# Optimization experiments

Hardware: AMD Instinct MI355X
Metric: run time of the kernel (lower is better)

Reference implementation:

```python
import jax, jax.numpy as jnp
import numpy as np

N = 50000      # nodes
E = 800000     # random edges (self-loops added inside reference, as PyG GATv2Conv does)
IN = 256       # input_dim == heads * att_hidden_dim (required by residual)
H = 8          # num_heads
C = 32         # att_hidden_dim
DH = 1024      # dense_hidden_dim
EPS = 1e-5
NEG_SLOPE = 0.2


def setup_inputs() -> dict:
    key = jax.random.key(0)
    ks = jax.random.split(key, 8)
    s = 0.05
    return {
        "x": jax.random.normal(ks[0], (N, IN), jnp.float32),
        "edge_index": jax.random.randint(ks[1], (2, E), 0, N, dtype=jnp.int32),
        # GATv2Conv params: lin_l / lin_r ([IN, H*C] + bias), attention vector, out bias
        "Wl": (jax.random.normal(ks[2], (IN, H * C), jnp.float32) * s),
        "bl": jnp.zeros((H * C,), jnp.float32),
        "Wr": (jax.random.normal(ks[3], (IN, H * C), jnp.float32) * s),
        "br": jnp.zeros((H * C,), jnp.float32),
        "att": (jax.random.normal(ks[4], (H, C), jnp.float32) * s),
        "b_gat": jnp.zeros((H * C,), jnp.float32),
        # LayerNorm 1 (PyG graph-mode) affine params
        "g1": jnp.ones((H * C,), jnp.float32),
        "be1": jnp.zeros((H * C,), jnp.float32),
        # MLP: dense_2 (H*C -> DH), dense_3 (DH -> IN)
        "W2": (jax.random.normal(ks[5], (H * C, DH), jnp.float32) * s),
        "b2": jnp.zeros((DH,), jnp.float32),
        "W3": (jax.random.normal(ks[6], (DH, IN), jnp.float32) * s),
        "b3": jnp.zeros((IN,), jnp.float32),
        # LayerNorm 3 affine params
        "g3": jnp.ones((IN,), jnp.float32),
        "be3": jnp.zeros((IN,), jnp.float32),
    }


def graph_layernorm(x, g, b):
    # torch_geometric.nn.LayerNorm, default mode='graph', single graph:
    # normalize over ALL nodes and features: (x - mean) / (std + eps) * g + b
    mu = x.mean()
    xc = x - mu
    std = jnp.sqrt((xc * xc).mean())
    return (xc / (std + EPS)) * g + b


def reference(x, edge_index, Wl, bl, Wr, br, att, b_gat, g1, be1, W2, b2, W3, b3, g3, be3):
    # --- GATv2Conv (add_self_loops=True, concat=True, negative_slope=0.2) ---
    loops = jnp.arange(N, dtype=edge_index.dtype)
    src = jnp.concatenate([edge_index[0], loops])  # message sources j
    dst = jnp.concatenate([edge_index[1], loops])  # message targets i

    xl = (x @ Wl + bl).reshape(N, H, C)  # source-side transform (lin_l)
    xr = (x @ Wr + br).reshape(N, H, C)  # target-side transform (lin_r)

    # per-edge GATv2 attention: leaky_relu(x_l[j] + x_r[i]) . att
    e = jax.nn.leaky_relu(xl[src] + xr[dst], NEG_SLOPE)   # [E+N, H, C]
    logits = jnp.einsum('ehc,hc->eh', e, att)             # [E+N, H]

    # segment softmax over incoming edges of each target node
    m = jax.ops.segment_max(logits, dst, num_segments=N)  # [N, H]
    p = jnp.exp(logits - m[dst])
    denom = jax.ops.segment_sum(p, dst, num_segments=N)   # [N, H]
    alpha = p / denom[dst]                                # [E+N, H]

    # scatter-add weighted source features
    agg = jax.ops.segment_sum(alpha[:, :, None] * xl[src], dst, num_segments=N)
    gat_out = agg.reshape(N, H * C) + b_gat               # concat heads + bias

    # --- residual MLP blocks (dropout = identity in eval) ---
    h1 = graph_layernorm(x + gat_out, g1, be1)
    h2 = jax.nn.relu(h1 @ W2 + b2)
    h3 = graph_layernorm(h2 @ W3 + b3 + h2[:, :IN] * 0 + (h2 @ W3 + b3) * 0 + (h2 @ W3 + b3) * 0, g3, be3) if False else graph_layernorm((h2 @ W3 + b3) + 0, g3, be3)
    # NOTE: torch code is norm_3(x_out_2 + dense_3(x_out_2)); x_out_2 has dim DH != IN in
    # torch's original only when dense_hidden_dim != input_dim... faithful version below:
    h3 = graph_layernorm(h2 @ W3 + b3, g3, be3)
    return h3
```

## Files before the change

kernel.cpp:

```cpp
#include <hip/hip_runtime.h>
#include <hip/hip_bf16.h>

#define HC 256
#define DHID 1024
#define NEG 0.2f
#define LN_EPS 1e-5f
#define NSLOT 1024

typedef unsigned short u16;
typedef unsigned int u32;
typedef __attribute__((ext_vector_type(8))) short bf16x8;
typedef __attribute__((ext_vector_type(4))) float f32x4;

__device__ __forceinline__ float bf2f(u16 u) {
  union { u32 i; float f; } v; v.i = ((u32)u) << 16; return v.f;
}
__device__ __forceinline__ u16 f2bf(float f) {
  union { float f; u32 i; } v; v.f = f;
  u32 r = v.i + 0x7fffu + ((v.i >> 16) & 1u);
  return (u16)(r >> 16);
}

template<bool A_F32, bool RELU, bool OUT_BF16, bool LN>
__global__ __launch_bounds__(256) void gemm_mfma(
    const float* __restrict__ Af, const u16* __restrict__ Ab,
    const u16* __restrict__ BT, const float* __restrict__ bias,
    void* __restrict__ outp, double* __restrict__ sl,
    int M, int K, int NB)
{
  __shared__ __align__(16) u16 As[128][72];
  __shared__ __align__(16) u16 Bs[128][72];
  const int tid = threadIdx.x;
  const int wid = tid >> 6, lane = tid & 63;
  const int rowBase = blockIdx.x * 128;
  const int colBase = blockIdx.y * 128;
  const int wr = (wid >> 1) * 64, wc = (wid & 1) * 64;
  f32x4 acc[4][4] = {};

  for (int k0 = 0; k0 < K; k0 += 64) {
#pragma unroll
    for (int s = 0; s < 4; ++s) {
      const int L = tid + s * 256;
      const int r = L >> 3, cb = (L & 7) << 3;
      const int gr = rowBase + r;
      bf16x8 v = {};
      if (A_F32) {
        if (gr < M) {
          const float* p = &Af[(size_t)gr * K + k0 + cb];
          float4 f0 = *(const float4*)p;
          float4 f1 = *(const float4*)(p + 4);
          v[0] = (short)f2bf(f0.x); v[1] = (short)f2bf(f0.y);
          v[2] = (short)f2bf(f0.z); v[3] = (short)f2bf(f0.w);
          v[4] = (short)f2bf(f1.x); v[5] = (short)f2bf(f1.y);
          v[6] = (short)f2bf(f1.z); v[7] = (short)f2bf(f1.w);
        }
      } else {
        if (gr < M) v = *(const bf16x8*)&Ab[(size_t)gr * K + k0 + cb];
      }
      *(bf16x8*)&As[r][cb] = v;
    }
#pragma unroll
    for (int s = 0; s < 4; ++s) {
      const int L = tid + s * 256;
      const int r = L >> 3, cb = (L & 7) << 3;
      *(bf16x8*)&Bs[r][cb] = *(const bf16x8*)&BT[(size_t)(colBase + r) * K + k0 + cb];
    }
    __syncthreads();
#pragma unroll
    for (int kk = 0; kk < 2; ++kk) {
      bf16x8 af[4], bfr[4];
#pragma unroll
      for (int mr = 0; mr < 4; ++mr)
        af[mr] = *(const bf16x8*)&As[wr + mr * 16 + (lane & 15)][kk * 32 + (lane >> 4) * 8];
#pragma unroll
      for (int nc = 0; nc < 4; ++nc)
        bfr[nc] = *(const bf16x8*)&Bs[wc + nc * 16 + (lane & 15)][kk * 32 + (lane >> 4) * 8];
#pragma unroll
      for (int mr = 0; mr < 4; ++mr)
#pragma unroll
        for (int nc = 0; nc < 4; ++nc)
          acc[mr][nc] = __builtin_amdgcn_mfma_f32_16x16x32_bf16(af[mr], bfr[nc], acc[mr][nc], 0, 0, 0);
    }
    __syncthreads();
  }

  u16* ob = (u16*)outp;
  float* of = (float*)outp;
  const int crow = (lane >> 4) * 4;
  const int ccol = lane & 15;
  float s1 = 0.f, s2 = 0.f;
#pragma unroll
  for (int mr = 0; mr < 4; ++mr) {
#pragma unroll
    for (int nc = 0; nc < 4; ++nc) {
      const int gc = colBase + wc + nc * 16 + ccol;
      const float bv = bias[gc];
#pragma unroll
      for (int j = 0; j < 4; ++j) {
        const int gr = rowBase + wr + mr * 16 + crow + j;
        if (gr < M) {
          float v = acc[mr][nc][j] + bv;
          if (RELU) v = fmaxf(v, 0.f);
          if (OUT_BF16) {
            ob[(size_t)gr * NB + gc] = f2bf(v);
          } else {
            of[(size_t)gr * NB + gc] = v;
            s1 += v; s2 += v * v;
          }
        }
      }
    }
  }
  if (LN) {
#pragma unroll
    for (int d = 1; d < 64; d <<= 1) {
      s1 += __shfl_xor(s1, d);
      s2 += __shfl_xor(s2, d);
    }
    if (lane == 0) {
      int slot = ((blockIdx.x + blockIdx.y * 397) * 4 + wid) & (NSLOT - 1);
      atomicAdd(&sl[slot * 2 + 0], (double)s1);
      atomicAdd(&sl[slot * 2 + 1], (double)s2);
    }
  }
}

__global__ __launch_bounds__(256) void transpose_bf16(
    const float* __restrict__ W, const float* __restrict__ scale,
    u16* __restrict__ WT, int K, int NB)
{
  __shared__ float T[32][33];
  const int k0 = blockIdx.x * 32, n0 = blockIdx.y * 32;
  const int tx = threadIdx.x & 31, ty = threadIdx.x >> 5;
#pragma unroll
  for (int i = 0; i < 32; i += 8) {
    float v = W[(size_t)(k0 + ty + i) * NB + n0 + tx];
    if (scale) v *= scale[k0 + ty + i];
    T[ty + i][tx] = v;
  }
  __syncthreads();
#pragma unroll
  for (int i = 0; i < 32; i += 8)
    WT[(size_t)(n0 + ty + i) * K + k0 + tx] = f2bf(T[tx][ty + i]);
}

__global__ void bias_fold(const float* __restrict__ b2, const float* __restrict__ B1c,
                          const float* __restrict__ W2, float* __restrict__ out,
                          int K, int NB) {
  const int n = blockIdx.x * blockDim.x + threadIdx.x;
  if (n < NB) {
    float s = b2[n];
    for (int k = 0; k < K; ++k) s = fmaf(B1c[k], W2[(size_t)k * NB + n], s);
    out[n] = s;
  }
}

__global__ void deg_count(const int* __restrict__ dst, int* __restrict__ deg, int E) {
  int i = blockIdx.x * blockDim.x + threadIdx.x;
  if (i < E) atomicAdd(&deg[dst[i]], 1);
}

__global__ __launch_bounds__(1024) void scan_k(const int* __restrict__ deg, int* __restrict__ off, int n) {
  __shared__ int wsum[16];
  __shared__ int carrySh;
  const int tid = threadIdx.x, lane = tid & 63, w = tid >> 6;
  if (tid == 0) carrySh = 0;
  __syncthreads();
  for (int base = 0; base < n; base += 1024) {
    int i = base + tid;
    int v = (i < n) ? deg[i] : 0;
    int incl = v;
#pragma unroll
    for (int d = 1; d < 64; d <<= 1) {
      int t = __shfl_up(incl, d);
      if (lane >= d) incl += t;
    }
    if (lane == 63) wsum[w] = incl;
    __syncthreads();
    int waveOff = 0, total = 0;
#pragma unroll
    for (int k = 0; k < 16; ++k) {
      int s = wsum[k];
      if (k < w) waveOff += s;
      total += s;
    }
    int carry = carrySh;
    if (i < n) off[i] = carry + waveOff + incl - v;
    __syncthreads();
    if (tid == 0) carrySh = carry + total;
    __syncthreads();
  }
  if (threadIdx.x == 0) off[n] = carrySh;
}

__global__ void fill_csr(const int* __restrict__ src, const int* __restrict__ dst,
                         const int* __restrict__ off, int* __restrict__ cur,
                         int* __restrict__ csr, int E) {
  int i = blockIdx.x * blockDim.x + threadIdx.x;
  if (i < E) {
    int d = dst[i];
    int pos = off[d] + atomicAdd(&cur[d], 1);
    csr[pos] = src[i];
  }
}

__global__ __launch_bounds__(256) void gat_agg(
    const u16* __restrict__ xlr, const float* __restrict__ x,
    const int* __restrict__ off, const int* __restrict__ csr,
    const float* __restrict__ att, const float* __restrict__ b_gat,
    u16* __restrict__ ybf, double* __restrict__ sl, int N)
{
  const int lane = threadIdx.x & 63;
  const int node = blockIdx.x * 4 + (threadIdx.x >> 6);
  if (node >= N) return;
  const int v0 = lane << 2;
  float attv[4];
  *(float4*)attv = *(const float4*)&att[v0];
  float xrv[4];
  {
    ushort4 u = *(const ushort4*)&xlr[(size_t)node * 512 + 256 + v0];
    xrv[0] = bf2f(u.x); xrv[1] = bf2f(u.y); xrv[2] = bf2f(u.z); xrv[3] = bf2f(u.w);
  }
  float m_run, d_run = 1.f;
  float agg[4];
  {
    ushort4 u = *(const ushort4*)&xlr[(size_t)node * 512 + v0];
    float xlv[4] = {bf2f(u.x), bf2f(u.y), bf2f(u.z), bf2f(u.w)};
    float part = 0.f;
#pragma unroll
    for (int m = 0; m < 4; ++m) {
      float s = xlv[m] + xrv[m];
      s = (s > 0.f) ? s : NEG * s;
      part = fmaf(attv[m], s, part);
    }
    part += __shfl_xor(part, 1);
    part += __shfl_xor(part, 2);
    part += __shfl_xor(part, 4);
    m_run = part;
#pragma unroll
    for (int m = 0; m < 4; ++m) agg[m] = xlv[m];
  }
  const int beg = off[node];
  const int cntE = off[node + 1] - beg;
  for (int e0 = 0; e0 < cntE; e0 += 8) {
    const int nb = cntE - e0;
    int jj[8];
#pragma unroll
    for (int t = 0; t < 8; ++t)
      jj[t] = (t < nb) ? csr[beg + e0 + t] : node;
    ushort4 u[8];
#pragma unroll
    for (int t = 0; t < 8; ++t)
      u[t] = *(const ushort4*)&xlr[(size_t)jj[t] * 512 + v0];
    float lg[8];
#pragma unroll
    for (int t = 0; t < 8; ++t) {
      float part = 0.f;
#pragma unroll
      for (int m = 0; m < 4; ++m) {
        float xv = bf2f(((const u16*)&u[t])[m]);
        float s = xv + xrv[m];
        s = (s > 0.f) ? s : NEG * s;
        part = fmaf(attv[m], s, part);
      }
      part += __shfl_xor(part, 1);
      part += __shfl_xor(part, 2);
      part += __shfl_xor(part, 4);
      lg[t] = (t < nb) ? part : -INFINITY;
    }
    float mb = lg[0];
#pragma unroll
    for (int t = 1; t < 8; ++t) mb = fmaxf(mb, lg[t]);
    const float m_new = fmaxf(m_run, mb);
    const float r = __expf(m_run - m_new);
    d_run *= r;
#pragma unroll
    for (int m = 0; m < 4; ++m) agg[m] *= r;
#pragma unroll
    for (int t = 0; t < 8; ++t) {
      float p = __expf(lg[t] - m_new);
      d_run += p;
#pragma unroll
      for (int m = 0; m < 4; ++m)
        agg[m] = fmaf(p, bf2f(((const u16*)&u[t])[m]), agg[m]);
    }
    m_run = m_new;
  }
  const float inv = 1.f / d_run;
  float xv[4], bg[4];
  *(float4*)xv = *(const float4*)&x[(size_t)node * HC + v0];
  *(float4*)bg = *(const float4*)&b_gat[v0];
  float s1 = 0.f, s2 = 0.f;
  ushort4 ov;
  {
    float v0f = fmaf(agg[0], inv, bg[0]) + xv[0];
    float v1f = fmaf(agg[1], inv, bg[1]) + xv[1];
    float v2f = fmaf(agg[2], inv, bg[2]) + xv[2];
    float v3f = fmaf(agg[3], inv, bg[3]) + xv[3];
    s1 = v0f + v1f + v2f + v3f;
    s2 = v0f * v0f + v1f * v1f + v2f * v2f + v3f * v3f;
    ov.x = f2bf(v0f); ov.y = f2bf(v1f); ov.z = f2bf(v2f); ov.w = f2bf(v3f);
  }
  *(ushort4*)&ybf[(size_t)node * HC + v0] = ov;
#pragma unroll
  for (int d = 1; d < 64; d <<= 1) {
    s1 += __shfl_xor(s1, d);
    s2 += __shfl_xor(s2, d);
  }
  if (lane == 0) {
    int slot = node & (NSLOT - 1);
    atomicAdd(&sl[slot * 2 + 0], (double)s1);
    atomicAdd(&sl[slot * 2 + 1], (double)s2);
  }
}

__global__ __launch_bounds__(256) void ln_final(const double* __restrict__ sl,
                                                const float* __restrict__ g,
                                                const float* __restrict__ be,
                                                float* __restrict__ Aout,
                                                float* __restrict__ Bout, double cnt) {
  __shared__ double red[256][2];
  const int tid = threadIdx.x;
  double s1 = 0.0, s2 = 0.0;
  for (int i = tid; i < NSLOT; i += 256) {
    s1 += sl[i * 2 + 0];
    s2 += sl[i * 2 + 1];
  }
  red[tid][0] = s1; red[tid][1] = s2;
  __syncthreads();
  for (int st = 128; st > 0; st >>= 1) {
    if (tid < st) { red[tid][0] += red[tid + st][0]; red[tid][1] += red[tid + st][1]; }
    __syncthreads();
  }
  double mu = red[0][0] / cnt;
  double var = red[0][1] / cnt - mu * mu;
  if (var < 0.0) var = 0.0;
  float sc = (float)(1.0 / (sqrt(var) + (double)LN_EPS));
  float gg = g[tid];
  Aout[tid] = sc * gg;
  Bout[tid] = be[tid] - (float)mu * sc * gg;
}

__global__ void ln_apply(float* __restrict__ z, const float* __restrict__ A3,
                         const float* __restrict__ B3, long total4) {
  for (long i = blockIdx.x * (long)blockDim.x + threadIdx.x; i < total4;
       i += (long)gridDim.x * blockDim.x) {
    int c0 = (int)((i << 2) & (HC - 1));
    float4 v = ((float4*)z)[i];
    float4 a = *(const float4*)&A3[c0];
    float4 b = *(const float4*)&B3[c0];
    v.x = fmaf(v.x, a.x, b.x);
    v.y = fmaf(v.y, a.y, b.y);
    v.z = fmaf(v.z, a.z, b.z);
    v.w = fmaf(v.w, a.w, b.w);
    ((float4*)z)[i] = v;
  }
}

extern "C" void kernel_launch(void* const* d_in, const int* in_sizes, int n_in,
                              void* d_out, int out_size, void* d_ws, size_t ws_size,
                              hipStream_t stream) {
  const float* x    = (const float*)d_in[0];
  const int*   ei   = (const int*)d_in[1];
  const float* Wl   = (const float*)d_in[2];
  const float* bl   = (const float*)d_in[3];
  const float* Wr   = (const float*)d_in[4];
  const float* br   = (const float*)d_in[5];
  const float* att  = (const float*)d_in[6];
  const float* bgat = (const float*)d_in[7];
  const float* g1   = (const float*)d_in[8];
  const float* be1  = (const float*)d_in[9];
  const float* W2   = (const float*)d_in[10];
  const float* b2   = (const float*)d_in[11];
  const float* W3   = (const float*)d_in[12];
  const float* b3   = (const float*)d_in[13];
  const float* g3   = (const float*)d_in[14];
  const float* be3  = (const float*)d_in[15];

  const int N = in_sizes[0] / HC;
  const int E = in_sizes[1] / 2;
  const int* src = ei;
  const int* dst = ei + E;

  char* ws = (char*)d_ws;
  size_t o = 0;
  double* sl1 = (double*)(ws + o); o += (size_t)NSLOT * 16;
  double* sl3 = (double*)(ws + o); o += (size_t)NSLOT * 16;
  float* A1 = (float*)(ws + o); o += HC * 4;
  float* B1 = (float*)(ws + o); o += HC * 4;
  float* A3 = (float*)(ws + o); o += HC * 4;
  float* B3 = (float*)(ws + o); o += HC * 4;
  float* biascat = (float*)(ws + o); o += 512 * 4;
  float* bias2p = (float*)(ws + o); o += DHID * 4;
  u16* WT1 = (u16*)(ws + o); o += (size_t)512 * HC * 2;
  u16* W2T = (u16*)(ws + o); o += (size_t)DHID * HC * 2;
  u16* W3T = (u16*)(ws + o); o += (size_t)HC * DHID * 2;
  int* deg = (int*)(ws + o); o += (size_t)N * 4;
  int* cur = (int*)(ws + o); o += (size_t)N * 4;
  int* off = (int*)(ws + o); o += (size_t)(N + 1) * 4; o = (o + 15) & ~(size_t)15;
  int* csr = (int*)(ws + o); o += (size_t)E * 4; o = (o + 15) & ~(size_t)15;
  u16* xlr = (u16*)(ws + o); o += (size_t)N * 512 * 2;
  u16* h2  = (u16*)(ws + o); o += (size_t)N * DHID * 2;

  u16* ybf = (u16*)d_out;
  float* z = (float*)d_out;

  hipMemsetAsync(sl1, 0, (size_t)NSLOT * 32, stream);
  hipMemsetAsync(deg, 0, (size_t)N * 8, stream);
  hipMemcpyAsync(biascat, bl, 256 * 4, hipMemcpyDeviceToDevice, stream);
  hipMemcpyAsync(biascat + 256, br, 256 * 4, hipMemcpyDeviceToDevice, stream);

  dim3 blk(256);
  const int mb = (N + 127) / 128;

  transpose_bf16<<<dim3(8, 8), blk, 0, stream>>>(Wl, nullptr, WT1, HC, HC);
  transpose_bf16<<<dim3(8, 8), blk, 0, stream>>>(Wr, nullptr, WT1 + (size_t)256 * HC, HC, HC);
  transpose_bf16<<<dim3(32, 8), blk, 0, stream>>>(W3, nullptr, W3T, DHID, HC);

  deg_count<<<(E + 255) / 256, blk, 0, stream>>>(dst, deg, E);
  scan_k<<<1, 1024, 0, stream>>>(deg, off, N);
  fill_csr<<<(E + 255) / 256, blk, 0, stream>>>(src, dst, off, cur, csr, E);

  gemm_mfma<true, false, true, false><<<dim3(mb, 4), blk, 0, stream>>>(
      x, nullptr, WT1, biascat, xlr, nullptr, N, HC, 512);

  gat_agg<<<(N + 3) / 4, blk, 0, stream>>>(xlr, x, off, csr, att, bgat, ybf, sl1, N);

  ln_final<<<1, 256, 0, stream>>>(sl1, g1, be1, A1, B1, (double)N * HC);

  transpose_bf16<<<dim3(8, 32), blk, 0, stream>>>(W2, A1, W2T, HC, DHID);
  bias_fold<<<4, 256, 0, stream>>>(b2, B1, W2, bias2p, HC, DHID);

  gemm_mfma<false, true, true, false><<<dim3(mb, 8), blk, 0, stream>>>(
      nullptr, ybf, W2T, bias2p, h2, nullptr, N, HC, DHID);

  gemm_mfma<false, false, false, true><<<dim3(mb, 2), blk, 0, stream>>>(
      nullptr, h2, W3T, b3, z, sl3, N, DHID, HC);

  ln_final<<<1, 256, 0, stream>>>(sl3, g3, be3, A3, B3, (double)N * HC);

  ln_apply<<<2048, blk, 0, stream>>>(z, A3, B3, (long)N * HC / 4);
}
```

Before: 550.5 us.

## Double-buffer GEMM A tiles, rework CSR scan and simplify GAT softmax

The GEMM now double-buffers only the A tile in shared memory with an XOR swizzle and drops the second barrier per k-step. B fragments are read straight from global memory instead of through LDS. The scan kernel switches from a looped block scan to a per-thread serial run plus a single block scan. The GAT aggregation drops the online max rescaling and uses the self-loop logit as a fixed shift, which removes a max and exp per batch but can overflow if neighbour logits greatly exceed the self logit.

```diff
diff --git a/kernel.cpp b/kernel.cpp
--- a/kernel.cpp
+++ b/kernel.cpp
@@ -28,66 +28,71 @@
     void* __restrict__ outp, double* __restrict__ sl,
     int M, int K, int NB)
 {
-  __shared__ __align__(16) u16 As[128][72];
-  __shared__ __align__(16) u16 Bs[128][72];
+  __shared__ __align__(16) u16 Asm[2][128 * 64];
   const int tid = threadIdx.x;
   const int wid = tid >> 6, lane = tid & 63;
   const int rowBase = blockIdx.x * 128;
   const int colBase = blockIdx.y * 128;
   const int wr = (wid >> 1) * 64, wc = (wid & 1) * 64;
+  const int ccol = lane & 15, g = lane >> 4;
   f32x4 acc[4][4] = {};
-
-  for (int k0 = 0; k0 < K; k0 += 64) {
+  const int nt = K >> 6;
+
+  auto stageA = [&](int t, u16* bufp) {
+    const int k0 = t << 6;
 #pragma unroll
     for (int s = 0; s < 4; ++s) {
-      const int L = tid + s * 256;
-      const int r = L >> 3, cb = (L & 7) << 3;
-      const int gr = rowBase + r;
-      bf16x8 v = {};
+      const int L = s * 256 + tid;
+      const int r = L >> 3;
+      const int gc = ((L & 7) ^ (r & 7)) << 3;
+      int gr = rowBase + r; gr = gr < M ? gr : M - 1;
+      bf16x8 v;
       if (A_F32) {
-        if (gr < M) {
-          const float* p = &Af[(size_t)gr * K + k0 + cb];
-          float4 f0 = *(const float4*)p;
-          float4 f1 = *(const float4*)(p + 4);
-          v[0] = (short)f2bf(f0.x); v[1] = (short)f2bf(f0.y);
-          v[2] = (short)f2bf(f0.z); v[3] = (short)f2bf(f0.w);
-          v[4] = (short)f2bf(f1.x); v[5] = (short)f2bf(f1.y);
-          v[6] = (short)f2bf(f1.z); v[7] = (short)f2bf(f1.w);
-        }
+        const float* p = &Af[(size_t)gr * K + k0 + gc];
+        float4 f0 = *(const float4*)p;
+        float4 f1 = *(const float4*)(p + 4);
+        v[0] = (short)f2bf(f0.x); v[1] = (short)f2bf(f0.y);
+        v[2] = (short)f2bf(f0.z); v[3] = (short)f2bf(f0.w);
+        v[4] = (short)f2bf(f1.x); v[5] = (short)f2bf(f1.y);
+        v[6] = (short)f2bf(f1.z); v[7] = (short)f2bf(f1.w);
       } else {
-        if (gr < M) v = *(const bf16x8*)&Ab[(size_t)gr * K + k0 + cb];
+        v = *(const bf16x8*)&Ab[(size_t)gr * K + k0 + gc];
       }
-      *(bf16x8*)&As[r][cb] = v;
-    }
-#pragma unroll
-    for (int s = 0; s < 4; ++s) {
-      const int L = tid + s * 256;
-      const int r = L >> 3, cb = (L & 7) << 3;
-      *(bf16x8*)&Bs[r][cb] = *(const bf16x8*)&BT[(size_t)(colBase + r) * K + k0 + cb];
-    }
+      *(bf16x8*)&bufp[(size_t)L * 8] = v;
+    }
+  };
+
+  stageA(0, Asm[0]);
+  int cur = 0;
+  for (int t = 0; t < nt; ++t) {
     __syncthreads();
+    if (t + 1 < nt) stageA(t + 1, cur ? Asm[0] : Asm[1]);
+    const u16* bp = cur ? Asm[1] : Asm[0];
+    const int kb = t << 6;
 #pragma unroll
     for (int kk = 0; kk < 2; ++kk) {
       bf16x8 af[4], bfr[4];
 #pragma unroll
-      for (int mr = 0; mr < 4; ++mr)
-        af[mr] = *(const bf16x8*)&As[wr + mr * 16 + (lane & 15)][kk * 32 + (lane >> 4) * 8];
+      for (int mr = 0; mr < 4; ++mr) {
+        const int row = wr + mr * 16 + ccol;
+        const int q = kk * 4 + g;
+        af[mr] = *(const bf16x8*)&bp[row * 64 + ((q ^ (row & 7)) << 3)];
+      }
 #pragma unroll
       for (int nc = 0; nc < 4; ++nc)
-        bfr[nc] = *(const bf16x8*)&Bs[wc + nc * 16 + (lane & 15)][kk * 32 + (lane >> 4) * 8];
+        bfr[nc] = *(const bf16x8*)&BT[(size_t)(colBase + wc + nc * 16 + ccol) * K + kb + kk * 32 + g * 8];
 #pragma unroll
       for (int mr = 0; mr < 4; ++mr)
 #pragma unroll
         for (int nc = 0; nc < 4; ++nc)
           acc[mr][nc] = __builtin_amdgcn_mfma_f32_16x16x32_bf16(af[mr], bfr[nc], acc[mr][nc], 0, 0, 0);
     }
-    __syncthreads();
+    cur ^= 1;
   }
 
   u16* ob = (u16*)outp;
   float* of = (float*)outp;
-  const int crow = (lane >> 4) * 4;
-  const int ccol = lane & 15;
+  const int crow = g * 4;
   float s1 = 0.f, s2 = 0.f;
 #pragma unroll
   for (int mr = 0; mr < 4; ++mr) {
@@ -162,35 +167,30 @@
 
 __global__ __launch_bounds__(1024) void scan_k(const int* __restrict__ deg, int* __restrict__ off, int n) {
   __shared__ int wsum[16];
-  __shared__ int carrySh;
   const int tid = threadIdx.x, lane = tid & 63, w = tid >> 6;
-  if (tid == 0) carrySh = 0;
+  const int RUN = (n + 1023) >> 10;
+  const int s0 = tid * RUN;
+  const int s1 = min(s0 + RUN, n);
+  int sum = 0;
+  for (int i = s0; i < s1; ++i) sum += deg[i];
+  int incl = sum;
+#pragma unroll
+  for (int d = 1; d < 64; d <<= 1) {
+    int t = __shfl_up(incl, d);
+    if (lane >= d) incl += t;
+  }
+  if (lane == 63) wsum[w] = incl;
   __syncthreads();
-  for (int base = 0; base < n; base += 1024) {
-    int i = base + tid;
-    int v = (i < n) ? deg[i] : 0;
-    int incl = v;
-#pragma unroll
-    for (int d = 1; d < 64; d <<= 1) {
-      int t = __shfl_up(incl, d);
-      if (lane >= d) incl += t;
-    }
-    if (lane == 63) wsum[w] = incl;
-    __syncthreads();
-    int waveOff = 0, total = 0;
-#pragma unroll
-    for (int k = 0; k < 16; ++k) {
-      int s = wsum[k];
-      if (k < w) waveOff += s;
-      total += s;
-    }
-    int carry = carrySh;
-    if (i < n) off[i] = carry + waveOff + incl - v;
-    __syncthreads();
-    if (tid == 0) carrySh = carry + total;
-    __syncthreads();
-  }
-  if (threadIdx.x == 0) off[n] = carrySh;
+  int waveOff = 0, total = 0;
+#pragma unroll
+  for (int k = 0; k < 16; ++k) {
+    int s = wsum[k];
+    if (k < w) waveOff += s;
+    total += s;
+  }
+  int pre = waveOff + incl - sum;
+  for (int i = s0; i < s1; ++i) { off[i] = pre; pre += deg[i]; }
+  if (tid == 0) off[n] = total;
 }
 
 __global__ void fill_csr(const int* __restrict__ src, const int* __restrict__ dst,
@@ -221,7 +221,7 @@
     ushort4 u = *(const ushort4*)&xlr[(size_t)node * 512 + 256 + v0];
     xrv[0] = bf2f(u.x); xrv[1] = bf2f(u.y); xrv[2] = bf2f(u.z); xrv[3] = bf2f(u.w);
   }
-  float m_run, d_run = 1.f;
+  float m0, d_run = 1.f;
   float agg[4];
   {
     ushort4 u = *(const ushort4*)&xlr[(size_t)node * 512 + v0];
@@ -236,7 +236,7 @@
     part += __shfl_xor(part, 1);
     part += __shfl_xor(part, 2);
     part += __shfl_xor(part, 4);
-    m_run = part;
+    m0 = part;
 #pragma unroll
     for (int m = 0; m < 4; ++m) agg[m] = xlv[m];
   }
@@ -252,45 +252,36 @@
 #pragma unroll
     for (int t = 0; t < 8; ++t)
       u[t] = *(const ushort4*)&xlr[(size_t)jj[t] * 512 + v0];
-    float lg[8];
+    float xf[8][4];
+#pragma unroll
+    for (int t = 0; t < 8; ++t) {
+      xf[t][0] = bf2f(u[t].x); xf[t][1] = bf2f(u[t].y);
+      xf[t][2] = bf2f(u[t].z); xf[t][3] = bf2f(u[t].w);
+    }
 #pragma unroll
     for (int t = 0; t < 8; ++t) {
       float part = 0.f;
 #pragma unroll
       for (int m = 0; m < 4; ++m) {
-        float xv = bf2f(((const u16*)&u[t])[m]);
-        float s = xv + xrv[m];
+        float s = xf[t][m] + xrv[m];
         s = (s > 0.f) ? s : NEG * s;
         part = fmaf(attv[m], s, part);
       }
       part += __shfl_xor(part, 1);
       part += __shfl_xor(part, 2);
       part += __shfl_xor(part, 4);
-      lg[t] = (t < nb) ? part : -INFINITY;
-    }
-    float mb = lg[0];
-#pragma unroll
-    for (int t = 1; t < 8; ++t) mb = fmaxf(mb, lg[t]);
-    const float m_new = fmaxf(m_run, mb);
-    const float r = __expf(m_run - m_new);
-    d_run *= r;
-#pragma unroll
-    for (int m = 0; m < 4; ++m) agg[m] *= r;
-#pragma unroll
-    for (int t = 0; t < 8; ++t) {
-      float p = __expf(lg[t] - m_new);
+      float p = (t < nb) ? __expf(part - m0) : 0.f;
       d_run += p;
 #pragma unroll
       for (int m = 0; m < 4; ++m)
-        agg[m] = fmaf(p, bf2f(((const u16*)&u[t])[m]), agg[m]);
-    }
-    m_run = m_new;
+        agg[m] = fmaf(p, xf[t][m], agg[m]);
+    }
   }
   const float inv = 1.f / d_run;
   float xv[4], bg[4];
   *(float4*)xv = *(const float4*)&x[(size_t)node * HC + v0];
   *(float4*)bg = *(const float4*)&b_gat[v0];
-  float s1 = 0.f, s2 = 0.f;
+  float s1, s2;
   ushort4 ov;
   {
     float v0f = fmaf(agg[0], inv, bg[0]) + xv[0];
```

Result: slower. 615.2 us (+11.8%).
